# Kernel tuning notes

Hardware: AMD Instinct MI355X
Metric: run time of the kernel (lower is better)

Reference implementation:

```python
import jax, jax.numpy as jnp
import numpy as np
from jax import lax

OUT_SIZE = 224  # original input spatial size (output_size of anomaly map)
NUM_NEIGHBORS = 9
SIGMA = 4.0
KSIZE = 2 * int(4.0 * SIGMA + 0.5) + 1  # 33, kornia-style kernel size


def avg_pool3(x):
    # AvgPool2d(3, 1, 1), count_include_pad=True -> sum over 3x3 window / 9
    s = lax.reduce_window(x, 0.0, lax.add, (1, 1, 3, 3), (1, 1, 1, 1),
                          [(0, 0), (0, 0), (1, 1), (1, 1)])
    return s / 9.0


def euclidean_dist(x, y):
    # x: [..., N, E], y: [..., M, E] -> [..., N, M]
    x_norm = jnp.sum(x * x, axis=-1, keepdims=True)
    y_norm = jnp.sum(y * y, axis=-1, keepdims=True)
    res = x_norm - 2.0 * jnp.matmul(x, jnp.swapaxes(y, -2, -1)) + jnp.swapaxes(y_norm, -2, -1)
    return jnp.sqrt(jnp.clip(res, 0.0))


def gaussian_blur(x):
    # x: [B,1,H,W]; separable Gaussian, reflect padding (kornia GaussianBlur2d default)
    r = KSIZE // 2
    t = jnp.arange(KSIZE, dtype=x.dtype) - r
    k = jnp.exp(-(t * t) / (2.0 * SIGMA * SIGMA))
    k = k / jnp.sum(k)
    xp = jnp.pad(x, ((0, 0), (0, 0), (r, r), (r, r)), mode='reflect')
    kh = k.reshape(1, 1, KSIZE, 1)
    kw = k.reshape(1, 1, 1, KSIZE)
    y = lax.conv_general_dilated(xp, kh, (1, 1), 'VALID',
                                 dimension_numbers=('NCHW', 'OIHW', 'NCHW'))
    return lax.conv_general_dilated(y, kw, (1, 1), 'VALID',
                                    dimension_numbers=('NCHW', 'OIHW', 'NCHW'))


def compute_anomaly_score(patch_scores, locations, embedding, memory_bank):
    # patch_scores/locations: [B, P]; embedding: [B*P, E]; memory_bank: [M, E]
    batch, num_patches = patch_scores.shape
    bidx = jnp.arange(batch)
    max_patches = jnp.argmax(patch_scores, axis=1)                       # [B]
    max_feats = embedding.reshape(batch, num_patches, -1)[bidx, max_patches]  # [B,E]
    score = patch_scores[bidx, max_patches]                              # [B]
    nn_index = locations[bidx, max_patches]                              # [B]
    nn_sample = memory_bank[nn_index]                                    # [B,E]
    n_nb = min(NUM_NEIGHBORS, memory_bank.shape[0])
    d_bank = euclidean_dist(nn_sample, memory_bank)                      # [B,M]
    _, support = lax.top_k(-d_bank, n_nb)                                # [B,k] smallest
    sup_feats = memory_bank[support]                                     # [B,k,E]
    d = euclidean_dist(max_feats[:, None, :], sup_feats)[:, 0, :]        # [B,k]
    weights = (1.0 - jax.nn.softmax(d, axis=1))[:, 0]                    # [B]
    return weights * score


def setup_inputs() -> dict:
    key = jax.random.key(0)
    k1, k2, k3 = jax.random.split(key, 3)
    feat2 = jax.random.normal(k1, (8, 512, 28, 28), dtype=jnp.float32)
    feat3 = jax.random.normal(k2, (8, 1024, 14, 14), dtype=jnp.float32)
    memory_bank = jax.random.normal(k3, (20000, 1536), dtype=jnp.float32)
    return {'feat2': feat2, 'feat3': feat3, 'memory_bank': memory_bank}


def reference(feat2, feat3, memory_bank):
    # feature pooling (AvgPool2d(3,1,1) on each backbone layer)
    f2 = avg_pool3(feat2)
    f3 = avg_pool3(feat3)
    batch, _, height, width = f2.shape
    # generate_embedding: bilinear upsample deeper layer, concat along channels
    f3u = jax.image.resize(f3, (batch, f3.shape[1], height, width), method='bilinear')
    emb = jnp.concatenate([f2, f3u], axis=1)                 # [B,1536,28,28]
    emb_dim = emb.shape[1]
    embedding = emb.transpose(0, 2, 3, 1).reshape(-1, emb_dim)  # [B*784, 1536]
    # nearest_neighbors with n_neighbors=1
    dist = euclidean_dist(embedding, memory_bank)            # [N, M]
    patch_scores = jnp.min(dist, axis=1)
    locations = jnp.argmin(dist, axis=1)
    patch_scores = patch_scores.reshape(batch, -1)
    locations = locations.reshape(batch, -1)
    pred_score = compute_anomaly_score(patch_scores, locations, embedding, memory_bank)
    # anomaly map: bilinear upsample patch scores to input size + gaussian blur
    score_map = patch_scores.reshape(batch, 1, width, height)
    amap = jax.image.resize(score_map, (batch, 1, OUT_SIZE, OUT_SIZE), method='bilinear')
    anomaly_map = gaussian_blur(amap)
    return anomaly_map, pred_score
```

## Files before the change

kernel.cpp:

```cpp
#include <hip/hip_runtime.h>
#include <math.h>

#define NB 8
#define C2 512
#define C3 1024
#define H2 28
#define W2 28
#define H3 14
#define W3 14
#define EDIM 1536
#define PPB (H2*W2)
#define NPATCH (NB*PPB)
#define MPAD 6400
#define MBANK 20000
#define OUTW 224
#define NNB 9
#define KS 33
#define KR 16
#define NMT 25
#define NNT 79
#define CHUNKS 8
#define CH (MBANK/CHUNKS)
#define MPB 64
#define NSLAB 24

#define SXQ 63.5f
#define SYQ (127.0f/6.0f)

typedef __attribute__((ext_vector_type(4))) int   i32x4;
typedef __attribute__((ext_vector_type(4))) float f32x4;

#define LEXLT(va,ia,vb,ib) ((va) < (vb) || ((va)==(vb) && (ia)<(ib)))
#define CSWAP(va,ia,vb,ib) { if (LEXLT(va,ia,vb,ib)) { float _tv=(vb); int _ti=(ib); (vb)=(va); (ib)=(ia); (va)=_tv; (ia)=_ti; } }

#define BAR() asm volatile("s_barrier" ::: "memory")
#define WAITV8() asm volatile("s_waitcnt vmcnt(8)" ::: "memory")
#define WAITV4() asm volatile("s_waitcnt vmcnt(4)" ::: "memory")
#define WAITV0() asm volatile("s_waitcnt vmcnt(0)" ::: "memory")

__device__ __forceinline__ void gload16(const void* g, void* l) {
  __builtin_amdgcn_global_load_lds(
      (const __attribute__((address_space(1))) unsigned int*)g,
      (__attribute__((address_space(3))) unsigned int*)l, 16, 0, 0);
}
__device__ __forceinline__ signed char q8(float x, float s) {
  int v = (int)rintf(x * s);
  v = v > 127 ? 127 : (v < -127 ? -127 : v);
  return (signed char)v;
}


__global__ __launch_bounds__(256) void pool2_kernel(const float* __restrict__ in,
    float* __restrict__ emb32, signed char* __restrict__ embq) {
  int bid = blockIdx.x;
  int cg = bid & 7; int h = (bid >> 3) % H2; int b = bid / (8*H2);
  int t = threadIdx.x;
  __shared__ float s3[3][64][29];
  for (int li = t; li < 3*64*28; li += 256) {
    int w = li % 28; int c = (li/28) & 63; int dh = li/(28*64);
    int hh = h + dh - 1;
    float v = 0.f;
    if (hh >= 0 && hh < H2) v = in[((size_t)(b*C2) + cg*64 + c)*784 + hh*28 + w];
    s3[dh][c][w] = v;
  }
  __syncthreads();
  for (int o = t; o < 64*28; o += 256) {
    int c = o & 63, w = o >> 6;
    float s = 0.f;
    #pragma unroll
    for (int dh = 0; dh < 3; ++dh) {
      s += s3[dh][c][w];
      if (w > 0)  s += s3[dh][c][w-1];
      if (w < 27) s += s3[dh][c][w+1];
    }
    s *= (1.f/9.f);
    size_t idx = ((size_t)(b*PPB) + h*28 + w)*EDIM + cg*64 + c;
    emb32[idx] = s;
    embq[idx] = q8(s, SXQ);
  }
}

__global__ void pool3_kernel(const float* __restrict__ in, float* __restrict__ f3p) {
  int id = blockIdx.x*blockDim.x + threadIdx.x;
  if (id >= NB*C3*H3*W3) return;
  int w = id % W3, h = (id / W3) % H3, c = (id / (H3*W3)) % C3, b = id / (C3*H3*W3);
  const float* src = in + (size_t)(b*C3 + c)*H3*W3;
  float s = 0.f;
  #pragma unroll
  for (int dh=-1; dh<=1; ++dh) {
    int hh = h+dh; if (hh<0||hh>=H3) continue;
    #pragma unroll
    for (int dw=-1; dw<=1; ++dw) {
      int ww = w+dw; if (ww<0||ww>=W3) continue;
      s += src[hh*W3+ww];
    }
  }
  f3p[(size_t)id] = s * (1.f/9.f);
}

__global__ __launch_bounds__(256) void up3_kernel(const float* __restrict__ f3p,
    float* __restrict__ emb32, signed char* __restrict__ embq) {
  int bid = blockIdx.x;
  int cg = bid & 15; int i = (bid >> 4) % H2; int b = bid / (16*H2);
  int t = threadIdx.x;
  float sy = i*0.5f - 0.25f; sy = fminf(fmaxf(sy,0.f),(float)(H3-1));
  int y0 = (int)sy; int y1 = min(y0+1,H3-1); float fy = sy - (float)y0;
  __shared__ float r2[2][64][15];
  for (int li = t; li < 2*64*14; li += 256) {
    int w = li % 14; int c = (li/14) & 63; int yy = li/(14*64);
    int ysrc = yy ? y1 : y0;
    r2[yy][c][w] = f3p[((size_t)(b*C3) + cg*64 + c)*196 + ysrc*14 + w];
  }
  __syncthreads();
  for (int o = t; o < 64*28; o += 256) {
    int c = o & 63, j = o >> 6;
    float sx = j*0.5f - 0.25f; sx = fminf(fmaxf(sx,0.f),(float)(W3-1));
    int x0 = (int)sx; int x1 = min(x0+1,W3-1); float fx = sx - (float)x0;
    float v = (1.f-fy)*((1.f-fx)*r2[0][c][x0] + fx*r2[0][c][x1])
            +      fy *((1.f-fx)*r2[1][c][x0] + fx*r2[1][c][x1]);
    size_t idx = ((size_t)(b*PPB) + i*28 + j)*EDIM + C2 + cg*64 + c;
    emb32[idx] = v;
    embq[idx] = q8(v, SXQ);
  }
}


__global__ void bank_prep_kernel(const float* __restrict__ bank, signed char* __restrict__ bankq,
                                 float* __restrict__ yn) {
  int w = (blockIdx.x*blockDim.x + threadIdx.x) >> 6;
  int lane = threadIdx.x & 63;
  if (w >= MBANK) return;
  const float4* p = reinterpret_cast<const float4*>(bank + (size_t)w*EDIM);
  int* q = reinterpret_cast<int*>(bankq + (size_t)w*EDIM);
  float acc = 0.f;
  #pragma unroll
  for (int k = 0; k < EDIM/4/64; ++k) {
    int k4 = lane + k*64;
    float4 v = p[k4];
    acc = fmaf(v.x,v.x,acc); acc = fmaf(v.y,v.y,acc);
    acc = fmaf(v.z,v.z,acc); acc = fmaf(v.w,v.w,acc);
    unsigned pk = ((unsigned)(unsigned char)q8(v.x, SYQ))
                | ((unsigned)(unsigned char)q8(v.y, SYQ) << 8)
                | ((unsigned)(unsigned char)q8(v.z, SYQ) << 16)
                | ((unsigned)(unsigned char)q8(v.w, SYQ) << 24);
    q[k4] = (int)pk;
  }
  #pragma unroll
  for (int s = 32; s; s >>= 1) acc += __shfl_xor(acc, s);
  if (lane == 0) yn[w] = acc;
}


__global__ __launch_bounds__(512, 2) void dist_min_i8(
    const signed char* __restrict__ A, const signed char* __restrict__ B,
    const float* __restrict__ yn, float* __restrict__ outq, int* __restrict__ outi)
{
  __shared__ __align__(16) unsigned char LDSC[131072];
  const int t = threadIdx.x;
  const int lane = t & 63, wid = t >> 6;
  const int wr = wid >> 2, wc = wid & 3;

  const int nwg = NMT*NNT;
  int orig = blockIdx.x;
  int xcd = orig & 7, loc = orig >> 3;
  int qq = nwg >> 3, rm = nwg & 7;
  int wg = (xcd < rm ? xcd*(qq+1) : rm*(qq+1) + (xcd-rm)*qq) + loc;
  const int mt = wg / NNT, nt = wg % NNT;
  const int m0 = mt*256, n0 = nt*256;

  const int l3 = lane >> 3, l7 = lane & 7;
  const int D = l7 ^ l3;
  const int koS = (D & 3) << 4;
  const int rhi = D >> 2;
  const int r0 = wid*32 + (l3<<1) + rhi;
  const int r1 = r0 + 16;
  const char* Ac = (const char*)A + (size_t)m0*EDIM;
  const char* Bc = (const char*)B;
  const unsigned aoff0 = (unsigned)(r0*EDIM + koS);
  const unsigned aoff1 = (unsigned)(r1*EDIM + koS);
  int bn0 = n0 + r0; bn0 = bn0 < MBANK ? bn0 : MBANK-1;
  int bn1 = n0 + r1; bn1 = bn1 < MBANK ? bn1 : MBANK-1;
  const unsigned boff0 = (unsigned)bn0*(unsigned)EDIM + (unsigned)koS;
  const unsigned boff1 = (unsigned)bn1*(unsigned)EDIM + (unsigned)koS;
  char* const dstBase = (char*)LDSC + (wid << 11);

  const int h = lane & 15, g = lane >> 4;
  const int csw = (((h & 1) << 2) | g) ^ (h >> 1);
  const unsigned abyte = (unsigned)(((wr*128 + h) >> 1)*128 + csw*16);
  const unsigned bbyte = (unsigned)(((wc*64 + h) >> 1)*128 + csw*16);

  i32x4 acc[8][4];
  #pragma unroll
  for (int i = 0; i < 8; ++i)
    #pragma unroll
    for (int j = 0; j < 4; ++j) acc[i][j] = (i32x4){0,0,0,0};

  #pragma unroll
  for (int s = 0; s < 3; ++s) {
    const unsigned sl = (unsigned)s*16384u;
    gload16(Ac + aoff0 + s*64, dstBase + sl);
    gload16(Ac + aoff1 + s*64, dstBase + sl + 1024);
    gload16(Bc + boff0 + s*64, dstBase + 65536u + sl);
    gload16(Bc + boff1 + s*64, dstBase + 65536u + sl + 1024);
  }
  WAITV8();
  BAR();

  #pragma unroll 4
  for (int p = 0; p < NSLAB; ++p) {
    const unsigned sA = (unsigned)(p & 3)*16384u;
    const unsigned sB = sA + 65536u;
    i32x4 af[8], bfv[4];
    #pragma unroll
    for (int j = 0; j < 4; ++j)
      bfv[j] = *(const i32x4*)(LDSC + sB + bbyte + j*1024);
    #pragma unroll
    for (int i = 0; i < 8; ++i)
      af[i] = *(const i32x4*)(LDSC + sA + abyte + i*1024);
    if (p < NSLAB-3) {
      const unsigned sW = (unsigned)((p+3) & 3)*16384u;
      gload16(Ac + aoff0 + (p+3)*64, dstBase + sW);
      gload16(Ac + aoff1 + (p+3)*64, dstBase + sW + 1024);
      gload16(Bc + boff0 + (p+3)*64, dstBase + 65536u + sW);
      gload16(Bc + boff1 + (p+3)*64, dstBase + 65536u + sW + 1024);
    }
    __builtin_amdgcn_s_setprio(1);
    #pragma unroll
    for (int i = 0; i < 8; ++i)
      #pragma unroll
      for (int j = 0; j < 4; ++j)
        acc[i][j] = __builtin_amdgcn_mfma_i32_16x16x64_i8(af[i], bfv[j], acc[i][j], 0, 0, 0);
    __builtin_amdgcn_s_setprio(0);
    if (p < NSLAB-3) { WAITV8(); }
    else if (p == NSLAB-3) { WAITV4(); }
    else if (p == NSLAB-2) { WAITV0(); }
    BAR();
  }

  const float NEG2INV = -2.0f * (2.0f/127.0f) * (6.0f/127.0f);
  float ynv[4];
  #pragma unroll
  for (int j = 0; j < 4; ++j) {
    int col = n0 + wc*64 + j*16 + h;
    ynv[j] = col < MBANK ? yn[col] : INFINITY;
  }
  float* smin = (float*)LDSC;
  int* sidx = (int*)(LDSC + 4096);
  #pragma unroll
  for (int i = 0; i < 8; ++i) {
    #pragma unroll
    for (int r = 0; r < 4; ++r) {
      float v = INFINITY; int ix = 0x7fffffff;
      #pragma unroll
      for (int j = 0; j < 4; ++j) {
        float q = fmaf(NEG2INV, (float)acc[i][j][r], ynv[j]);
        int col = n0 + wc*64 + j*16 + h;
        if (q < v || (q == v && col < ix)) { v = q; ix = col; }
      }
      #pragma unroll
      for (int m = 1; m < 16; m <<= 1) {
        float ov = __shfl_xor(v, m);
        int   oi = __shfl_xor(ix, m);
        if (ov < v || (ov == v && oi < ix)) { v = ov; ix = oi; }
      }
      if (h == 0) {
        int rl = wr*128 + i*16 + g*4 + r;
        smin[rl*4 + wc] = v;
        sidx[rl*4 + wc] = ix;
      }
    }
  }
  __syncthreads();
  if (t < 256) {
    float v = smin[t*4]; int ix = sidx[t*4];
    #pragma unroll
    for (int w = 1; w < 4; ++w) {
      float ov = smin[t*4+w]; int oi = sidx[t*4+w];
      if (ov < v || (ov == v && oi < ix)) { v = ov; ix = oi; }
    }
    int row = m0 + t;
    if (row < NPATCH) {
      outq[(size_t)nt*NPATCH + row] = v;
      outi[(size_t)nt*NPATCH + row] = ix;
    }
  }
}

__global__ void reduce_min_kernel(const float* __restrict__ outq, const int* __restrict__ outi,
                                  int* __restrict__ loc) {
  int r = blockIdx.x*blockDim.x + threadIdx.x;
  if (r >= NPATCH) return;
  float bv = INFINITY; int bi = 0x7fffffff;
  for (int s = 0; s < NNT; ++s) {
    float v = outq[(size_t)s*NPATCH + r];
    int  ix = outi[(size_t)s*NPATCH + r];
    if (v < bv || (v == bv && ix < bi)) { bv = v; bi = ix; }
  }
  loc[r] = bi;
}

__global__ void rescore_kernel(const float* __restrict__ emb32, const float* __restrict__ bank,
                               const float* __restrict__ yn,
                               const int* __restrict__ loc, float* __restrict__ ps) {
  int w = (blockIdx.x*blockDim.x + threadIdx.x) >> 6;
  int lane = threadIdx.x & 63;
  if (w >= NPATCH) return;
  int j = loc[w];
  const float4* x = reinterpret_cast<const float4*>(emb32 + (size_t)w*EDIM);
  const float4* y = reinterpret_cast<const float4*>(bank + (size_t)j*EDIM);
  float accd = 0.f, accx = 0.f;
  #pragma unroll
  for (int k = 0; k < EDIM/4/64; ++k) {
    float4 a = x[lane + k*64], b = y[lane + k*64];
    accd = fmaf(a.x,b.x,accd); accd = fmaf(a.y,b.y,accd);
    accd = fmaf(a.z,b.z,accd); accd = fmaf(a.w,b.w,accd);
    accx = fmaf(a.x,a.x,accx); accx = fmaf(a.y,a.y,accx);
    accx = fmaf(a.z,a.z,accx); accx = fmaf(a.w,a.w,accx);
  }
  #pragma unroll
  for (int s = 32; s; s >>= 1) { accd += __shfl_xor(accd, s); accx += __shfl_xor(accx, s); }
  if (lane == 0) ps[w] = sqrtf(fmaxf(accx - 2.f*accd + yn[j], 0.f));
}


__global__ void argmax_kernel(const float* __restrict__ ps, const int* __restrict__ loc,
                              float* __restrict__ bscore, int* __restrict__ brow, int* __restrict__ bnn) {
  __shared__ float sv[256]; __shared__ int si[256];
  int b = blockIdx.x, t = threadIdx.x;
  float bv = -INFINITY; int bi = 0x7fffffff;
  for (int p = t; p < PPB; p += 256) {
    float v = ps[b*PPB + p];
    if (v > bv || (v == bv && p < bi)) { bv = v; bi = p; }
  }
  sv[t] = bv; si[t] = bi; __syncthreads();
  for (int s = 128; s; s >>= 1) {
    if (t < s) {
      if (sv[t+s] > sv[t] || (sv[t+s] == sv[t] && si[t+s] < si[t])) { sv[t] = sv[t+s]; si[t] = si[t+s]; }
    }
    __syncthreads();
  }
  if (t == 0) {
    bscore[b] = sv[0];
    brow[b]   = b*PPB + si[0];
    bnn[b]    = loc[b*PPB + si[0]];
  }
}

__global__ __launch_bounds__(256) void dbank_kernel(
    const signed char* __restrict__ bankq, const float* __restrict__ yn,
    const int* __restrict__ bnn, float* __restrict__ dbank)
{
  __shared__ float xs[8][EDIM];
  int t = threadIdx.x;
  for (int idx = t*16; idx < 8*EDIM; idx += 256*16) {
    int b = idx / EDIM, k = idx % EDIM;
    int4 v = *reinterpret_cast<const int4*>(bankq + (size_t)bnn[b]*EDIM + k);
    const signed char* pc = (const signed char*)&v;
    #pragma unroll
    for (int e = 0; e < 16; ++e) xs[b][k+e] = (float)pc[e];
  }
  __syncthreads();
  const float INV2 = 1.0f / (SYQ*SYQ);
  int lane = t & 63, w = t >> 6;
  for (int u = 0; u < MPB/4; ++u) {
    int m = blockIdx.x*MPB + u*4 + w;
    if (m < MBANK) {
      const int4* yp = reinterpret_cast<const int4*>(bankq + (size_t)m*EDIM);
      float acc[8] = {0.f,0.f,0.f,0.f,0.f,0.f,0.f,0.f};
      for (int k16 = lane; k16 < EDIM/16; k16 += 64) {
        int4 y = yp[k16];
        const signed char* yc = (const signed char*)&y;
        int k = k16*16;
        #pragma unroll
        for (int b = 0; b < 8; ++b) {
          float a = 0.f;
          #pragma unroll
          for (int e = 0; e < 16; ++e) a = fmaf((float)yc[e], xs[b][k+e], a);
          acc[b] += a;
        }
      }
      #pragma unroll
      for (int b = 0; b < 8; ++b) {
        float a = acc[b];
        #pragma unroll
        for (int s = 32; s; s >>= 1) a += __shfl_xor(a, s);
        acc[b] = a;
      }
      if (lane == 0) {
        #pragma unroll
        for (int b = 0; b < 8; ++b) {
          int nn = bnn[b];
          float d2 = yn[nn] - 2.f*acc[b]*INV2 + yn[m];
          dbank[(size_t)b*MBANK + m] = sqrtf(fmaxf(d2, 0.f));
        }
      }
    }
  }
}


__global__ __launch_bounds__(256) void top9_stage1(const float* __restrict__ dbank,
                                                   float* __restrict__ cv, int* __restrict__ ci) {
  int b = blockIdx.x / CHUNKS, ch = blockIdx.x % CHUNKS;
  const float* db = dbank + (size_t)b*MBANK + ch*CH;
  int t = threadIdx.x;

  float v0=INFINITY,v1=INFINITY,v2=INFINITY,v3=INFINITY,v4=INFINITY,
        v5=INFINITY,v6=INFINITY,v7=INFINITY,v8=INFINITY;
  int i0=0x7fffffff,i1=0x7fffffff,i2=0x7fffffff,i3=0x7fffffff,i4=0x7fffffff,
      i5=0x7fffffff,i6=0x7fffffff,i7=0x7fffffff,i8=0x7fffffff;

  for (int s = 0; s < (CH+255)/256; ++s) {
    int m = t + s*256;
    if (m < CH) {
      float nv = db[m]; int ni = ch*CH + m;
      if (LEXLT(nv,ni,v8,i8)) {
        v8 = nv; i8 = ni;
        CSWAP(v8,i8,v7,i7); CSWAP(v7,i7,v6,i6); CSWAP(v6,i6,v5,i5); CSWAP(v5,i5,v4,i4);
        CSWAP(v4,i4,v3,i3); CSWAP(v3,i3,v2,i2); CSWAP(v2,i2,v1,i1); CSWAP(v1,i1,v0,i0);
      }
    }
  }

  __shared__ float sv[256*9];
  __shared__ int   si[256*9];
  __shared__ float rv[256]; __shared__ int ri[256]; __shared__ int rp[256];
  sv[t*9+0]=v0; sv[t*9+1]=v1; sv[t*9+2]=v2; sv[t*9+3]=v3; sv[t*9+4]=v4;
  sv[t*9+5]=v5; sv[t*9+6]=v6; sv[t*9+7]=v7; sv[t*9+8]=v8;
  si[t*9+0]=i0; si[t*9+1]=i1; si[t*9+2]=i2; si[t*9+3]=i3; si[t*9+4]=i4;
  si[t*9+5]=i5; si[t*9+6]=i6; si[t*9+7]=i7; si[t*9+8]=i8;
  __syncthreads();

  for (int r = 0; r < NNB; ++r) {
    float bv = INFINITY; int bix = 0x7fffffff; int bp = -1;
    #pragma unroll
    for (int u = 0; u < 9; ++u) {
      float v = sv[t*9+u]; int ix = si[t*9+u];
      if (LEXLT(v,ix,bv,bix)) { bv = v; bix = ix; bp = t*9+u; }
    }
    rv[t] = bv; ri[t] = bix; rp[t] = bp; __syncthreads();
    for (int s = 128; s; s >>= 1) {
      if (t < s) {
        if (LEXLT(rv[t+s],ri[t+s],rv[t],ri[t])) { rv[t]=rv[t+s]; ri[t]=ri[t+s]; rp[t]=rp[t+s]; }
      }
      __syncthreads();
    }
    if (t == 0) {
      cv[blockIdx.x*NNB + r] = rv[0];
      ci[blockIdx.x*NNB + r] = ri[0];
      sv[rp[0]] = INFINITY; si[rp[0]] = 0x7fffffff;
    }
    __syncthreads();
  }
}


__global__ void top9_stage2(const float* __restrict__ cv, const int* __restrict__ ci,
                            int* __restrict__ support) {
  __shared__ float sv[128]; __shared__ int si[128];
  __shared__ float wv[128]; __shared__ int wi[128]; __shared__ int wp[128];
  int b = blockIdx.x, t = threadIdx.x;
  if (t < CHUNKS*NNB) { sv[t] = cv[b*CHUNKS*NNB + t]; si[t] = ci[b*CHUNKS*NNB + t]; }
  else { sv[t] = INFINITY; si[t] = 0x7fffffff; }
  __syncthreads();
  for (int r = 0; r < NNB; ++r) {
    wv[t] = sv[t]; wi[t] = si[t]; wp[t] = t; __syncthreads();
    for (int s = 64; s; s >>= 1) {
      if (t < s) {
        if (LEXLT(wv[t+s],wi[t+s],wv[t],wi[t])) { wv[t]=wv[t+s]; wi[t]=wi[t+s]; wp[t]=wp[t+s]; }
      }
      __syncthreads();
    }
    if (t == 0) {
      support[b*NNB + r] = wi[0];
      sv[wp[0]] = INFINITY; si[wp[0]] = 0x7fffffff;
    }
    __syncthreads();
  }
}

__global__ void dsup_kernel(const float* __restrict__ emb32, const float* __restrict__ bank,
                            const float* __restrict__ yn,
                            const int* __restrict__ brow, const int* __restrict__ support,
                            float* __restrict__ dsup) {
  int w = (blockIdx.x*blockDim.x + threadIdx.x) >> 6;
  int lane = threadIdx.x & 63;
  if (w >= NB*NNB) return;
  int b = w / NNB, j = w % NNB;
  int row = brow[b]; int sup = support[b*NNB + j];
  const float* x = emb32 + (size_t)row*EDIM;
  const float* y = bank + (size_t)sup*EDIM;
  float accd = 0.f, accx = 0.f;
  for (int k = lane; k < EDIM; k += 64) {
    float a = x[k];
    accd = fmaf(a, y[k], accd);
    accx = fmaf(a, a, accx);
  }
  #pragma unroll
  for (int s = 32; s; s >>= 1) { accd += __shfl_xor(accd, s); accx += __shfl_xor(accx, s); }
  if (lane == 0) dsup[b*NNB + j] = sqrtf(fmaxf(accx - 2.f*accd + yn[sup], 0.f));
}

__global__ void pred_kernel(const float* __restrict__ dsup, const float* __restrict__ bscore,
                            float* __restrict__ out) {
  int b = threadIdx.x;
  if (b >= NB) return;
  float d[NNB]; float mx = -INFINITY;
  #pragma unroll
  for (int j = 0; j < NNB; ++j) { d[j] = dsup[b*NNB + j]; mx = fmaxf(mx, d[j]); }
  float s = 0.f;
  #pragma unroll
  for (int j = 0; j < NNB; ++j) s += expf(d[j] - mx);
  float w = 1.f - expf(d[0] - mx) / s;
  out[b] = w * bscore[b];
}


__device__ __forceinline__ int refl224(int x) {
  if (x < 0) return -x;
  if (x > OUTW-1) return 2*(OUTW-1) - x;
  return x;
}

__global__ __launch_bounds__(256) void upblurh_kernel(const float* __restrict__ ps,
                                                      float* __restrict__ tmp) {
  int b = blockIdx.x / OUTW, i = blockIdx.x % OUTW;
  int t = threadIdx.x;
  __shared__ float l[W2];
  __shared__ float graw[KS];
  if (t < KS) {
    float x = (float)t - (float)KR;
    graw[t] = expf(-(x*x) / (2.f*4.f*4.f));
  }
  float sy = ((float)i + 0.5f)*0.125f - 0.5f; sy = fminf(fmaxf(sy,0.f),(float)(H2-1));
  int y0 = (int)sy; int y1 = min(y0+1,H2-1); float fy = sy - (float)y0;
  if (t < W2) {
    const float* p = ps + b*PPB;
    l[t] = (1.f-fy)*p[y0*W2+t] + fy*p[y1*W2+t];
  }
  __syncthreads();
  if (t >= OUTW) return;
  float gsum = 0.f;
  #pragma unroll
  for (int u = 0; u < KS; ++u) gsum += graw[u];
  float winv = 1.f / gsum;
  float s = 0.f;
  #pragma unroll
  for (int v = 0; v < KS; ++v) {
    int jj = refl224(t - KR + v);
    float sx = ((float)jj + 0.5f)*0.125f - 0.5f; sx = fminf(fmaxf(sx,0.f),(float)(W2-1));
    int x0 = (int)sx; int x1 = min(x0+1,W2-1); float fx = sx - (float)x0;
    s = fmaf(graw[v]*winv, (1.f-fx)*l[x0] + fx*l[x1], s);
  }
  tmp[((size_t)b*OUTW + i)*OUTW + t] = s;
}

__global__ __launch_bounds__(256) void blurv_kernel(const float* __restrict__ in,
                                                    float* __restrict__ out) {
  __shared__ float graw[KS];
  int t = threadIdx.x;
  if (t < KS) {
    float x = (float)t - (float)KR;
    graw[t] = expf(-(x*x) / (2.f*4.f*4.f));
  }
  __syncthreads();
  int id = blockIdx.x*blockDim.x + t;
  if (id >= NB*OUTW*OUTW) return;
  float gsum = 0.f;
  #pragma unroll
  for (int u = 0; u < KS; ++u) gsum += graw[u];
  float winv = 1.f / gsum;
  int j = id % OUTW, i = (id/OUTW) % OUTW, b = id/(OUTW*OUTW);
  float s = 0.f;
  #pragma unroll
  for (int u = 0; u < KS; ++u) {
    int ii = refl224(i - KR + u);
    s = fmaf(graw[u]*winv, in[((size_t)b*OUTW + ii)*OUTW + j], s);
  }
  out[id] = s;
}


extern "C" void kernel_launch(void* const* d_in, const int* in_sizes, int n_in,
                              void* d_out, int out_size, void* d_ws, size_t ws_size,
                              hipStream_t stream) {
  const float* feat2 = (const float*)d_in[0];
  const float* feat3 = (const float*)d_in[1];
  const float* bank  = (const float*)d_in[2];
  float* out = (float*)d_out;

  char* base = (char*)d_ws;
  size_t off = 0;
  auto alloc = [&](size_t nbytes) -> char* {
    char* p = base + off;
    off += ((nbytes + 255) & ~(size_t)255);
    return p;
  };
  float*       emb32 = (float*)      alloc((size_t)NPATCH*EDIM*4);
  signed char* embq  = (signed char*)alloc((size_t)MPAD*EDIM);
  signed char* bankq = (signed char*)alloc((size_t)MBANK*EDIM);
  float* f3p    = (float*)alloc((size_t)NB*C3*H3*W3*4);
  float* yn     = (float*)alloc(MBANK*4);
  float* outq   = (float*)alloc((size_t)NNT*NPATCH*4);
  int*   outi   = (int*)  alloc((size_t)NNT*NPATCH*4);
  float* ps     = (float*)alloc(NPATCH*4);
  int*   loc    = (int*)  alloc(NPATCH*4);
  float* bscore = (float*)alloc(NB*4);
  int*   brow   = (int*)  alloc(NB*4);
  int*   bnn    = (int*)  alloc(NB*4);
  float* dbank  = (float*)alloc((size_t)NB*MBANK*4);
  float* cv     = (float*)alloc(NB*CHUNKS*NNB*4);
  int*   ci     = (int*)  alloc(NB*CHUNKS*NNB*4);
  int*   supp   = (int*)  alloc(NB*NNB*4);
  float* dsup   = (float*)alloc(NB*NNB*4);
  float* tmp    = (float*)alloc((size_t)NB*OUTW*OUTW*4);

  pool2_kernel<<<NB*H2*8, 256, 0, stream>>>(feat2, emb32, embq);
  {
    int n = NB*C3*H3*W3;
    pool3_kernel<<<(n+255)/256, 256, 0, stream>>>(feat3, f3p);
  }
  up3_kernel<<<NB*H2*16, 256, 0, stream>>>(f3p, emb32, embq);
  bank_prep_kernel<<<(MBANK*64)/256, 256, 0, stream>>>(bank, bankq, yn);

  dist_min_i8<<<NMT*NNT, 512, 0, stream>>>(embq, bankq, yn, outq, outi);
  reduce_min_kernel<<<(NPATCH+255)/256, 256, 0, stream>>>(outq, outi, loc);
  rescore_kernel<<<(NPATCH*64)/256, 256, 0, stream>>>(emb32, bank, yn, loc, ps);

  argmax_kernel<<<NB, 256, 0, stream>>>(ps, loc, bscore, brow, bnn);
  dbank_kernel<<<(MBANK+MPB-1)/MPB, 256, 0, stream>>>(bankq, yn, bnn, dbank);
  top9_stage1<<<NB*CHUNKS, 256, 0, stream>>>(dbank, cv, ci);
  top9_stage2<<<NB, 128, 0, stream>>>(cv, ci, supp);
  dsup_kernel<<<(NB*NNB*64 + 255)/256, 256, 0, stream>>>(emb32, bank, yn, brow, supp, dsup);
  pred_kernel<<<1, 64, 0, stream>>>(dsup, bscore, out + NB*OUTW*OUTW);

  {
    upblurh_kernel<<<NB*OUTW, 256, 0, stream>>>(ps, tmp);
    int n = NB*OUTW*OUTW;
    blurv_kernel<<<(n+255)/256, 256, 0, stream>>>(tmp, out);
  }
}
```

Baseline: 561.7 us.

## Shrink int8 distance GEMM tile, use fp32 bank distances, fuse final kernels

The int8 distance-min GEMM moves from 256x256 tiles with a 4-stage LDS pipeline to 256x128 tiles with double buffering and 48KB LDS. This targets higher occupancy (4 blocks per CU) and doubles the N-tile count reduced afterward. The bank-distance kernel now uses the fp32 bank instead of the quantized copy, which improves precision but reads four times the bytes. The top-9 selection, support distances and prediction kernels are fused into one finalize kernel to cut launch overhead. The new GEMM pipeline waits on all loads every slab, so it may hide less global-memory latency.

After: 542.6 us. 3.4% less time.

```diff
diff --git a/kernel.cpp b/kernel.cpp
--- a/kernel.cpp
+++ b/kernel.cpp
@@ -18,7 +18,7 @@
 #define KS 33
 #define KR 16
 #define NMT 25
-#define NNT 79
+#define NNTB 157
 #define CHUNKS 8
 #define CH (MBANK/CHUNKS)
 #define MPB 64
@@ -28,14 +28,11 @@
 #define SYQ (127.0f/6.0f)
 
 typedef __attribute__((ext_vector_type(4))) int   i32x4;
-typedef __attribute__((ext_vector_type(4))) float f32x4;
 
 #define LEXLT(va,ia,vb,ib) ((va) < (vb) || ((va)==(vb) && (ia)<(ib)))
 #define CSWAP(va,ia,vb,ib) { if (LEXLT(va,ia,vb,ib)) { float _tv=(vb); int _ti=(ib); (vb)=(va); (ib)=(ia); (va)=_tv; (ia)=_ti; } }
 
 #define BAR() asm volatile("s_barrier" ::: "memory")
-#define WAITV8() asm volatile("s_waitcnt vmcnt(8)" ::: "memory")
-#define WAITV4() asm volatile("s_waitcnt vmcnt(4)" ::: "memory")
 #define WAITV0() asm volatile("s_waitcnt vmcnt(0)" ::: "memory")
 
 __device__ __forceinline__ void gload16(const void* g, void* l) {
@@ -151,89 +148,80 @@
 }
 
 
-__global__ __launch_bounds__(512, 2) void dist_min_i8(
+__global__ __launch_bounds__(512, 4) void dist_min_i8(
     const signed char* __restrict__ A, const signed char* __restrict__ B,
     const float* __restrict__ yn, float* __restrict__ outq, int* __restrict__ outi)
 {
-  __shared__ __align__(16) unsigned char LDSC[131072];
+  __shared__ __align__(16) unsigned char LDSC[49152];
   const int t = threadIdx.x;
   const int lane = t & 63, wid = t >> 6;
-  const int wr = wid >> 2, wc = wid & 3;
-
-  const int nwg = NMT*NNT;
+  const int wr = wid >> 1, wc = wid & 1;
+
+  const int nwg = NMT*NNTB;
   int orig = blockIdx.x;
   int xcd = orig & 7, loc = orig >> 3;
   int qq = nwg >> 3, rm = nwg & 7;
   int wg = (xcd < rm ? xcd*(qq+1) : rm*(qq+1) + (xcd-rm)*qq) + loc;
-  const int mt = wg / NNT, nt = wg % NNT;
-  const int m0 = mt*256, n0 = nt*256;
+  const int mt = wg / NNTB, nt = wg % NNTB;
+  const int m0 = mt*256, n0 = nt*128;
 
   const int l3 = lane >> 3, l7 = lane & 7;
   const int D = l7 ^ l3;
   const int koS = (D & 3) << 4;
   const int rhi = D >> 2;
-  const int r0 = wid*32 + (l3<<1) + rhi;
-  const int r1 = r0 + 16;
+  const int rA0 = wid*32 + (l3<<1) + rhi;
+  const int rA1 = rA0 + 16;
+  const int rB  = wid*16 + (l3<<1) + rhi;
   const char* Ac = (const char*)A + (size_t)m0*EDIM;
   const char* Bc = (const char*)B;
-  const unsigned aoff0 = (unsigned)(r0*EDIM + koS);
-  const unsigned aoff1 = (unsigned)(r1*EDIM + koS);
-  int bn0 = n0 + r0; bn0 = bn0 < MBANK ? bn0 : MBANK-1;
-  int bn1 = n0 + r1; bn1 = bn1 < MBANK ? bn1 : MBANK-1;
-  const unsigned boff0 = (unsigned)bn0*(unsigned)EDIM + (unsigned)koS;
-  const unsigned boff1 = (unsigned)bn1*(unsigned)EDIM + (unsigned)koS;
-  char* const dstBase = (char*)LDSC + (wid << 11);
+  const unsigned aoff0 = (unsigned)(rA0*EDIM + koS);
+  const unsigned aoff1 = (unsigned)(rA1*EDIM + koS);
+  int bn = n0 + rB; bn = bn < MBANK ? bn : MBANK-1;
+  const unsigned boff = (unsigned)bn*(unsigned)EDIM + (unsigned)koS;
+  char* const aDst = (char*)LDSC + wid*2048;
+  char* const bDst = (char*)LDSC + 16384 + wid*1024;
 
   const int h = lane & 15, g = lane >> 4;
   const int csw = (((h & 1) << 2) | g) ^ (h >> 1);
-  const unsigned abyte = (unsigned)(((wr*128 + h) >> 1)*128 + csw*16);
-  const unsigned bbyte = (unsigned)(((wc*64 + h) >> 1)*128 + csw*16);
-
-  i32x4 acc[8][4];
-  #pragma unroll
-  for (int i = 0; i < 8; ++i)
+  const unsigned abyte = (unsigned)(wr*4096 + (h>>1)*128 + csw*16);
+  const unsigned bbyte = (unsigned)(16384 + wc*4096 + (h>>1)*128 + csw*16);
+
+  i32x4 acc[4][4];
+  #pragma unroll
+  for (int i = 0; i < 4; ++i)
     #pragma unroll
     for (int j = 0; j < 4; ++j) acc[i][j] = (i32x4){0,0,0,0};
 
-  #pragma unroll
-  for (int s = 0; s < 3; ++s) {
-    const unsigned sl = (unsigned)s*16384u;
-    gload16(Ac + aoff0 + s*64, dstBase + sl);
-    gload16(Ac + aoff1 + s*64, dstBase + sl + 1024);
-    gload16(Bc + boff0 + s*64, dstBase + 65536u + sl);
-    gload16(Bc + boff1 + s*64, dstBase + 65536u + sl + 1024);
-  }
-  WAITV8();
+  gload16(Ac + aoff0, aDst);
+  gload16(Ac + aoff1, aDst + 1024);
+  gload16(Bc + boff,  bDst);
+  WAITV0();
   BAR();
 
-  #pragma unroll 4
+  #pragma unroll 2
   for (int p = 0; p < NSLAB; ++p) {
-    const unsigned sA = (unsigned)(p & 3)*16384u;
-    const unsigned sB = sA + 65536u;
-    i32x4 af[8], bfv[4];
+    const unsigned sb = (unsigned)(p & 1)*24576u;
+    if (p < NSLAB-1) {
+      const unsigned sw = (unsigned)((p+1) & 1)*24576u;
+      gload16(Ac + aoff0 + (p+1)*64, aDst + sw);
+      gload16(Ac + aoff1 + (p+1)*64, aDst + sw + 1024);
+      gload16(Bc + boff  + (p+1)*64, bDst + sw);
+    }
+    i32x4 af[4], bfv[4];
     #pragma unroll
     for (int j = 0; j < 4; ++j)
-      bfv[j] = *(const i32x4*)(LDSC + sB + bbyte + j*1024);
-    #pragma unroll
-    for (int i = 0; i < 8; ++i)
-      af[i] = *(const i32x4*)(LDSC + sA + abyte + i*1024);
-    if (p < NSLAB-3) {
-      const unsigned sW = (unsigned)((p+3) & 3)*16384u;
-      gload16(Ac + aoff0 + (p+3)*64, dstBase + sW);
-      gload16(Ac + aoff1 + (p+3)*64, dstBase + sW + 1024);
-      gload16(Bc + boff0 + (p+3)*64, dstBase + 65536u + sW);
-      gload16(Bc + boff1 + (p+3)*64, dstBase + 65536u + sW + 1024);
-    }
+      bfv[j] = *(const i32x4*)(LDSC + sb + bbyte + j*1024);
+    #pragma unroll
+    for (int i = 0; i < 4; ++i)
+      af[i] = *(const i32x4*)(LDSC + sb + abyte + i*1024);
     __builtin_amdgcn_s_setprio(1);
     #pragma unroll
-    for (int i = 0; i < 8; ++i)
+    for (int i = 0; i < 4; ++i)
       #pragma unroll
       for (int j = 0; j < 4; ++j)
         acc[i][j] = __builtin_amdgcn_mfma_i32_16x16x64_i8(af[i], bfv[j], acc[i][j], 0, 0, 0);
     __builtin_amdgcn_s_setprio(0);
-    if (p < NSLAB-3) { WAITV8(); }
-    else if (p == NSLAB-3) { WAITV4(); }
-    else if (p == NSLAB-2) { WAITV0(); }
+    WAITV0();
     BAR();
   }
 
@@ -245,9 +233,9 @@
     ynv[j] = col < MBANK ? yn[col] : INFINITY;
   }
   float* smin = (float*)LDSC;
-  int* sidx = (int*)(LDSC + 4096);
-  #pragma unroll
-  for (int i = 0; i < 8; ++i) {
+  int* sidx = (int*)(LDSC + 2048);
+  #pragma unroll
+  for (int i = 0; i < 4; ++i) {
     #pragma unroll
     for (int r = 0; r < 4; ++r) {
       float v = INFINITY; int ix = 0x7fffffff;
@@ -264,20 +252,18 @@
         if (ov < v || (ov == v && oi < ix)) { v = ov; ix = oi; }
       }
       if (h == 0) {
-        int rl = wr*128 + i*16 + g*4 + r;
-        smin[rl*4 + wc] = v;
-        sidx[rl*4 + wc] = ix;
+        int rl = wr*64 + i*16 + g*4 + r;
+        smin[rl*2 + wc] = v;
+        sidx[rl*2 + wc] = ix;
       }
     }
   }
   __syncthreads();
   if (t < 256) {
-    float v = smin[t*4]; int ix = sidx[t*4];
-    #pragma unroll
-    for (int w = 1; w < 4; ++w) {
-      float ov = smin[t*4+w]; int oi = sidx[t*4+w];
-      if (ov < v || (ov == v && oi < ix)) { v = ov; ix = oi; }
-    }
+    float v0 = smin[t*2], v1 = smin[t*2+1];
+    int   i0 = sidx[t*2], i1 = sidx[t*2+1];
+    float v; int ix;
+    if (LEXLT(v1, i1, v0, i0)) { v = v1; ix = i1; } else { v = v0; ix = i0; }
     int row = m0 + t;
     if (row < NPATCH) {
       outq[(size_t)nt*NPATCH + row] = v;
@@ -291,7 +277,7 @@
   int r = blockIdx.x*blockDim.x + threadIdx.x;
   if (r >= NPATCH) return;
   float bv = INFINITY; int bi = 0x7fffffff;
-  for (int s = 0; s < NNT; ++s) {
+  for (int s = 0; s < NNTB; ++s) {
     float v = outq[(size_t)s*NPATCH + r];
     int  ix = outi[(size_t)s*NPATCH + r];
     if (v < bv || (v == bv && ix < bi)) { bv = v; bi = ix; }
@@ -347,36 +333,32 @@
 }
 
 __global__ __launch_bounds__(256) void dbank_kernel(
-    const signed char* __restrict__ bankq, const float* __restrict__ yn,
+    const float* __restrict__ bank, const float* __restrict__ yn,
     const int* __restrict__ bnn, float* __restrict__ dbank)
 {
   __shared__ float xs[8][EDIM];
   int t = threadIdx.x;
-  for (int idx = t*16; idx < 8*EDIM; idx += 256*16) {
+  for (int idx = t*4; idx < 8*EDIM; idx += 256*4) {
     int b = idx / EDIM, k = idx % EDIM;
-    int4 v = *reinterpret_cast<const int4*>(bankq + (size_t)bnn[b]*EDIM + k);
-    const signed char* pc = (const signed char*)&v;
-    #pragma unroll
-    for (int e = 0; e < 16; ++e) xs[b][k+e] = (float)pc[e];
-  }
-  __syncthreads();
-  const float INV2 = 1.0f / (SYQ*SYQ);
+    float4 v = *reinterpret_cast<const float4*>(bank + (size_t)bnn[b]*EDIM + k);
+    *reinterpret_cast<float4*>(&xs[b][k]) = v;
+  }
+  __syncthreads();
   int lane = t & 63, w = t >> 6;
   for (int u = 0; u < MPB/4; ++u) {
     int m = blockIdx.x*MPB + u*4 + w;
     if (m < MBANK) {
-      const int4* yp = reinterpret_cast<const int4*>(bankq + (size_t)m*EDIM);
+      const float4* yp = reinterpret_cast<const float4*>(bank + (size_t)m*EDIM);
       float acc[8] = {0.f,0.f,0.f,0.f,0.f,0.f,0.f,0.f};
-      for (int k16 = lane; k16 < EDIM/16; k16 += 64) {
-        int4 y = yp[k16];
-        const signed char* yc = (const signed char*)&y;
-        int k = k16*16;
+      for (int k4 = lane; k4 < EDIM/4; k4 += 64) {
+        float4 y = yp[k4];
+        int k = k4*4;
         #pragma unroll
         for (int b = 0; b < 8; ++b) {
-          float a = 0.f;
-          #pragma unroll
-          for (int e = 0; e < 16; ++e) a = fmaf((float)yc[e], xs[b][k+e], a);
-          acc[b] += a;
+          acc[b] = fmaf(y.x, xs[b][k+0], acc[b]);
+          acc[b] = fmaf(y.y, xs[b][k+1], acc[b]);
+          acc[b] = fmaf(y.z, xs[b][k+2], acc[b]);
+          acc[b] = fmaf(y.w, xs[b][k+3], acc[b]);
         }
       }
       #pragma unroll
@@ -390,7 +372,7 @@
         #pragma unroll
         for (int b = 0; b < 8; ++b) {
           int nn = bnn[b];
-          float d2 = yn[nn] - 2.f*acc[b]*INV2 + yn[m];
+          float d2 = yn[nn] - 2.f*acc[b] + yn[m];
           dbank[(size_t)b*MBANK + m] = sqrtf(fmaxf(d2, 0.f));
         }
       }
@@ -455,10 +437,14 @@
 }
 
 
-__global__ void top9_stage2(const float* __restrict__ cv, const int* __restrict__ ci,
-                            int* __restrict__ support) {
+__global__ __launch_bounds__(128) void finalize_kernel(
+    const float* __restrict__ cv, const int* __restrict__ ci,
+    const float* __restrict__ emb32, const float* __restrict__ bank,
+    const float* __restrict__ yn, const int* __restrict__ brow,
+    const float* __restrict__ bscore, float* __restrict__ out) {
   __shared__ float sv[128]; __shared__ int si[128];
   __shared__ float wv[128]; __shared__ int wi[128]; __shared__ int wp[128];
+  __shared__ int supp[NNB]; __shared__ float ds[NNB];
   int b = blockIdx.x, t = threadIdx.x;
   if (t < CHUNKS*NNB) { sv[t] = cv[b*CHUNKS*NNB + t]; si[t] = ci[b*CHUNKS*NNB + t]; }
   else { sv[t] = INFINITY; si[t] = 0x7fffffff; }
@@ -472,47 +458,37 @@
       __syncthreads();
     }
     if (t == 0) {
-      support[b*NNB + r] = wi[0];
+      supp[r] = wi[0];
       sv[wp[0]] = INFINITY; si[wp[0]] = 0x7fffffff;
     }
     __syncthreads();
   }
-}
-
-__global__ void dsup_kernel(const float* __restrict__ emb32, const float* __restrict__ bank,
-                            const float* __restrict__ yn,
-                            const int* __restrict__ brow, const int* __restrict__ support,
-                            float* __restrict__ dsup) {
-  int w = (blockIdx.x*blockDim.x + threadIdx.x) >> 6;
-  int lane = threadIdx.x & 63;
-  if (w >= NB*NNB) return;
-  int b = w / NNB, j = w % NNB;
-  int row = brow[b]; int sup = support[b*NNB + j];
+  int lane = t & 63, w = t >> 6;
+  int row = brow[b];
   const float* x = emb32 + (size_t)row*EDIM;
-  const float* y = bank + (size_t)sup*EDIM;
-  float accd = 0.f, accx = 0.f;
-  for (int k = lane; k < EDIM; k += 64) {
-    float a = x[k];
-    accd = fmaf(a, y[k], accd);
-    accx = fmaf(a, a, accx);
-  }
-  #pragma unroll
-  for (int s = 32; s; s >>= 1) { accd += __shfl_xor(accd, s); accx += __shfl_xor(accx, s); }
-  if (lane == 0) dsup[b*NNB + j] = sqrtf(fmaxf(accx - 2.f*accd + yn[sup], 0.f));
-}
-
-__global__ void pred_kernel(const float* __restrict__ dsup, const float* __restrict__ bscore,
-                            float* __restrict__ out) {
-  int b = threadIdx.x;
-  if (b >= NB) return;
-  float d[NNB]; float mx = -INFINITY;
-  #pragma unroll
-  for (int j = 0; j < NNB; ++j) { d[j] = dsup[b*NNB + j]; mx = fmaxf(mx, d[j]); }
-  float s = 0.f;
-  #pragma unroll
-  for (int j = 0; j < NNB; ++j) s += expf(d[j] - mx);
-  float w = 1.f - expf(d[0] - mx) / s;
-  out[b] = w * bscore[b];
+  for (int j = w; j < NNB; j += 2) {
+    const float* y = bank + (size_t)supp[j]*EDIM;
+    float accd = 0.f, accx = 0.f;
+    for (int k = lane; k < EDIM; k += 64) {
+      float a = x[k];
+      accd = fmaf(a, y[k], accd);
+      accx = fmaf(a, a, accx);
+    }
+    #pragma unroll
+    for (int s = 32; s; s >>= 1) { accd += __shfl_xor(accd, s); accx += __shfl_xor(accx, s); }
+    if (lane == 0) ds[j] = sqrtf(fmaxf(accx - 2.f*accd + yn[supp[j]], 0.f));
+  }
+  __syncthreads();
+  if (t == 0) {
+    float mx = -INFINITY;
+    #pragma unroll
+    for (int j = 0; j < NNB; ++j) mx = fmaxf(mx, ds[j]);
+    float s = 0.f;
+    #pragma unroll
+    for (int j = 0; j < NNB; ++j) s += expf(ds[j] - mx);
+    float wgt = 1.f - expf(ds[0] - mx) / s;
+    out[b] = wgt * bscore[b];
+  }
 }
 
 
@@ -601,8 +577,8 @@
   signed char* bankq = (signed char*)alloc((size_t)MBANK*EDIM);
   float* f3p    = (float*)alloc((size_t)NB*C3*H3*W3*4);
   float* yn     = (float*)alloc(MBANK*4);
-  float* outq   = (float*)alloc((size_t)NNT*NPATCH*4);
-  int*   outi   = (int*)  alloc((size_t)NNT*NPATCH*4);
+  float* outq   = (float*)alloc((size_t)NNTB*NPATCH*4);
+  int*   outi   = (int*)  alloc((size_t)NNTB*NPATCH*4);
   float* ps     = (float*)alloc(NPATCH*4);
   int*   loc    = (int*)  alloc(NPATCH*4);
   float* bscore = (float*)alloc(NB*4);
@@ -611,8 +587,6 @@
   float* dbank  = (float*)alloc((size_t)NB*MBANK*4);
   float* cv     = (float*)alloc(NB*CHUNKS*NNB*4);
   int*   ci     = (int*)  alloc(NB*CHUNKS*NNB*4);
-  int*   supp   = (int*)  alloc(NB*NNB*4);
-  float* dsup   = (float*)alloc(NB*NNB*4);
   float* tmp    = (float*)alloc((size_t)NB*OUTW*OUTW*4);
 
   pool2_kernel<<<NB*H2*8, 256, 0, stream>>>(feat2, emb32, embq);
@@ -623,16 +597,15 @@
   up3_kernel<<<NB*H2*16, 256, 0, stream>>>(f3p, emb32, embq);
   bank_prep_kernel<<<(MBANK*64)/256, 256, 0, stream>>>(bank, bankq, yn);
 
-  dist_min_i8<<<NMT*NNT, 512, 0, stream>>>(embq, bankq, yn, outq, outi);
+  dist_min_i8<<<NMT*NNTB, 512, 0, stream>>>(embq, bankq, yn, outq, outi);
   reduce_min_kernel<<<(NPATCH+255)/256, 256, 0, stream>>>(outq, outi, loc);
   rescore_kernel<<<(NPATCH*64)/256, 256, 0, stream>>>(emb32, bank, yn, loc, ps);
 
   argmax_kernel<<<NB, 256, 0, stream>>>(ps, loc, bscore, brow, bnn);
-  dbank_kernel<<<(MBANK+MPB-1)/MPB, 256, 0, stream>>>(bankq, yn, bnn, dbank);
+  dbank_kernel<<<(MBANK+MPB-1)/MPB, 256, 0, stream>>>(bank, yn, bnn, dbank);
   top9_stage1<<<NB*CHUNKS, 256, 0, stream>>>(dbank, cv, ci);
-  top9_stage2<<<NB, 128, 0, stream>>>(cv, ci, supp);
-  dsup_kernel<<<(NB*NNB*64 + 255)/256, 256, 0, stream>>>(emb32, bank, yn, brow, supp, dsup);
-  pred_kernel<<<1, 64, 0, stream>>>(dsup, bscore, out + NB*OUTW*OUTW);
+  finalize_kernel<<<NB, 128, 0, stream>>>(cv, ci, emb32, bank, yn, brow, bscore,
+                                          out + NB*OUTW*OUTW);
 
   {
     upblurh_kernel<<<NB*OUTW, 256, 0, stream>>>(ps, tmp);
```
